# Optimization experiments

Hardware: AMD Instinct MI355X
Metric: run time of the kernel (lower is better)

Reference implementation:

```python
import jax, jax.numpy as jnp
import numpy as np

B, P, E, D = 256, 2048, 16, 2
HID, OUT = 128, 128
BN_EPS = 1e-5


def setup_inputs() -> dict:
    key = jax.random.key(0)
    ks = jax.random.split(key, 16)
    inp = {
        "barcode_h0": jax.random.normal(ks[0], (B, P, D), jnp.float32),
        "barcode_h0_count": jax.random.randint(ks[1], (B,), 0, P),
        "barcode_h1": jax.random.normal(ks[2], (B, P, D), jnp.float32),
        "barcode_h1_count": jax.random.randint(ks[3], (B,), 0, P),
        # SLayer params (one per homology dim): centers ~ U[0,1), log_sharpness = log(3.0)
        "centers0": jax.random.uniform(ks[4], (E, D), jnp.float32),
        "log_sharp0": jnp.full((E, D), np.log(3.0), jnp.float32),
        "centers1": jax.random.uniform(ks[5], (E, D), jnp.float32),
        "log_sharp1": jnp.full((E, D), np.log(3.0), jnp.float32),
        # head: Linear(2E -> HID, no bias), BN, ReLU, Linear(HID -> OUT, no bias), BN
        "W1": jax.random.normal(ks[6], (2 * E, HID), jnp.float32) / np.sqrt(2 * E),
        "gamma1": jnp.ones((HID,), jnp.float32),
        "beta1": jnp.zeros((HID,), jnp.float32),
        "W2": jax.random.normal(ks[7], (HID, OUT), jnp.float32) / np.sqrt(HID),
        "gamma2": jnp.ones((OUT,), jnp.float32),
        "beta2": jnp.zeros((OUT,), jnp.float32),
    }
    return inp


def _slayer(pts, counts, centers, log_sharp):
    # pts: [B,P,2], counts: [B], centers/log_sharp: [E,2]
    sharp = jax.nn.softplus(log_sharp) + 1e-6                       # [E,2]
    diff = pts[:, :, None, :] - centers[None, None, :, :]           # [B,P,E,2]
    resp = jnp.exp(-jnp.sum(sharp * diff * diff, axis=-1))          # [B,P,E]
    mask = (jnp.arange(pts.shape[1])[None, :] < counts[:, None]).astype(resp.dtype)
    return jnp.sum(resp * mask[:, :, None], axis=1)                 # [B,E]


def _batchnorm_train(x, gamma, beta):
    m = jnp.mean(x, axis=0)
    v = jnp.var(x, axis=0)  # biased, as torch uses for normalization
    return (x - m) * jax.lax.rsqrt(v + BN_EPS) * gamma + beta


def reference(barcode_h0, barcode_h0_count, barcode_h1, barcode_h1_count,
              centers0, log_sharp0, centers1, log_sharp1,
              W1, gamma1, beta1, W2, gamma2, beta2):
    f0 = _slayer(barcode_h0, barcode_h0_count, centers0, log_sharp0)  # [B,E]
    f1 = _slayer(barcode_h1, barcode_h1_count, centers1, log_sharp1)  # [B,E]
    x = jnp.concatenate([f0, f1], axis=1)                             # [B,2E]
    h = jax.nn.relu(_batchnorm_train(x @ W1, gamma1, beta1))          # [B,HID]
    y = _batchnorm_train(h @ W2, gamma2, beta2)                       # [B,OUT]
    norm = jnp.maximum(jnp.linalg.norm(y, axis=1, keepdims=True), 1e-12)
    return y / norm
```

## Files before the change

### kernel.cpp

```cpp
#include <hip/hip_runtime.h>

#define Bsz 256
#define Pn  2048
#define En  16
#define HIDn 128
#define OUTn 128
#define BN_EPS 1e-5f

__global__ __launch_bounds__(256) void k_slayer_w1(
    const float* __restrict__ pts0, const int* __restrict__ cnt0,
    const float* __restrict__ pts1, const int* __restrict__ cnt1,
    const float* __restrict__ c0, const float* __restrict__ ls0,
    const float* __restrict__ c1, const float* __restrict__ ls1,
    const float* __restrict__ W1,
    float* __restrict__ u, float* __restrict__ sum1, float* __restrict__ sumsq1)
{
    __shared__ float cen[2][En][2];
    __shared__ float shp[2][En][2];
    __shared__ float red[4][32];
    __shared__ float xrow[32];

    const int tid = threadIdx.x;
    const int b   = blockIdx.x;

    if (tid < 64) {
        int h = tid >> 5, r = tid & 31, e = r >> 1, d = r & 1;
        const float* C = h ? c1 : c0;
        const float* L = h ? ls1 : ls0;
        cen[h][e][d] = C[e * 2 + d];
        float z  = L[e * 2 + d];
        float sp = (z > 20.f) ? z : logf(1.f + expf(z));
        shp[h][e][d] = sp + 1e-6f;
    }
    __syncthreads();

    float acc0[En], acc1[En];
    #pragma unroll
    for (int e = 0; e < En; e++) { acc0[e] = 0.f; acc1[e] = 0.f; }

    const int n0 = cnt0[b];
    const int n1 = cnt1[b];
    const float2* p0 = (const float2*)pts0 + (size_t)b * Pn;
    const float2* p1 = (const float2*)pts1 + (size_t)b * Pn;

    for (int p = tid; p < n0; p += 256) {
        float2 pt = p0[p];
        #pragma unroll
        for (int e = 0; e < En; e++) {
            float dx = pt.x - cen[0][e][0];
            float dy = pt.y - cen[0][e][1];
            float t  = shp[0][e][0] * dx * dx + shp[0][e][1] * dy * dy;
            acc0[e] += __expf(-t);
        }
    }
    for (int p = tid; p < n1; p += 256) {
        float2 pt = p1[p];
        #pragma unroll
        for (int e = 0; e < En; e++) {
            float dx = pt.x - cen[1][e][0];
            float dy = pt.y - cen[1][e][1];
            float t  = shp[1][e][0] * dx * dx + shp[1][e][1] * dy * dy;
            acc1[e] += __expf(-t);
        }
    }

    #pragma unroll
    for (int e = 0; e < En; e++) {
        #pragma unroll
        for (int off = 32; off > 0; off >>= 1) {
            acc0[e] += __shfl_down(acc0[e], off, 64);
            acc1[e] += __shfl_down(acc1[e], off, 64);
        }
    }
    const int wave = tid >> 6, lane = tid & 63;
    if (lane == 0) {
        #pragma unroll
        for (int e = 0; e < En; e++) { red[wave][e] = acc0[e]; red[wave][16 + e] = acc1[e]; }
    }
    __syncthreads();
    if (tid < 32) xrow[tid] = red[0][tid] + red[1][tid] + red[2][tid] + red[3][tid];
    __syncthreads();

    if (tid < HIDn) {
        float a = 0.f;
        #pragma unroll
        for (int k = 0; k < 32; k++) a = fmaf(xrow[k], W1[k * HIDn + tid], a);
        u[b * HIDn + tid] = a;
        atomicAdd(&sum1[tid], a);
        atomicAdd(&sumsq1[tid], a * a);
    }
}

__global__ __launch_bounds__(128) void k_bn1_w2(
    const float* __restrict__ u, const float* __restrict__ W2,
    const float* __restrict__ g1, const float* __restrict__ be1,
    const float* __restrict__ sum1, const float* __restrict__ sumsq1,
    float* __restrict__ ypre, float* __restrict__ sum2, float* __restrict__ sumsq2)
{
    __shared__ float hrow[HIDn];
    const int j = threadIdx.x, b = blockIdx.x;

    float uv   = u[b * HIDn + j];
    float m    = sum1[j] * (1.f / Bsz);
    float var  = sumsq1[j] * (1.f / Bsz) - m * m;
    float rstd = rsqrtf(var + BN_EPS);
    float h    = fmaxf((uv - m) * rstd * g1[j] + be1[j], 0.f);
    hrow[j] = h;
    __syncthreads();

    float a = 0.f;
    #pragma unroll 8
    for (int k = 0; k < HIDn; k++) a = fmaf(hrow[k], W2[k * OUTn + j], a);

    ypre[b * OUTn + j] = a;
    atomicAdd(&sum2[j], a);
    atomicAdd(&sumsq2[j], a * a);
}

__global__ __launch_bounds__(128) void k_bn2_norm(
    const float* __restrict__ ypre,
    const float* __restrict__ g2, const float* __restrict__ be2,
    const float* __restrict__ sum2, const float* __restrict__ sumsq2,
    float* __restrict__ out)
{
    __shared__ float part[2];
    const int j = threadIdx.x, b = blockIdx.x;

    float yv   = ypre[b * OUTn + j];
    float m    = sum2[j] * (1.f / Bsz);
    float var  = sumsq2[j] * (1.f / Bsz) - m * m;
    float rstd = rsqrtf(var + BN_EPS);
    float y    = (yv - m) * rstd * g2[j] + be2[j];

    float sq = y * y;
    #pragma unroll
    for (int off = 32; off > 0; off >>= 1) sq += __shfl_down(sq, off, 64);
    if ((j & 63) == 0) part[j >> 6] = sq;
    __syncthreads();
    float total = part[0] + part[1];
    float norm  = fmaxf(sqrtf(total), 1e-12f);
    out[b * OUTn + j] = y / norm;
}

extern "C" void kernel_launch(void* const* d_in, const int* in_sizes, int n_in,
                              void* d_out, int out_size, void* d_ws, size_t ws_size,
                              hipStream_t stream) {
    const float* pts0 = (const float*)d_in[0];
    const int*   cnt0 = (const int*)  d_in[1];
    const float* pts1 = (const float*)d_in[2];
    const int*   cnt1 = (const int*)  d_in[3];
    const float* c0   = (const float*)d_in[4];
    const float* ls0  = (const float*)d_in[5];
    const float* c1   = (const float*)d_in[6];
    const float* ls1  = (const float*)d_in[7];
    const float* W1   = (const float*)d_in[8];
    const float* g1   = (const float*)d_in[9];
    const float* be1  = (const float*)d_in[10];
    const float* W2   = (const float*)d_in[11];
    const float* g2   = (const float*)d_in[12];
    const float* be2  = (const float*)d_in[13];
    float* out = (float*)d_out;

    float* ws     = (float*)d_ws;
    float* u      = ws;
    float* ypre   = ws + 32768;
    float* sum1   = ws + 65536;
    float* sumsq1 = sum1 + 128;
    float* sum2   = sumsq1 + 128;
    float* sumsq2 = sum2 + 128;

    hipMemsetAsync(sum1, 0, 512 * sizeof(float), stream);

    k_slayer_w1<<<Bsz, 256, 0, stream>>>(pts0, cnt0, pts1, cnt1,
                                         c0, ls0, c1, ls1, W1,
                                         u, sum1, sumsq1);
    k_bn1_w2<<<Bsz, 128, 0, stream>>>(u, W2, g1, be1, sum1, sumsq1,
                                      ypre, sum2, sumsq2);
    k_bn2_norm<<<Bsz, 128, 0, stream>>>(ypre, g2, be2, sum2, sumsq2, out);
}
```

Measured before the change: 106.9 us.

## Fuse three kernels into one cooperative kernel with grid syncs

```diff
diff --git a/kernel.cpp b/kernel.cpp
--- a/kernel.cpp
+++ b/kernel.cpp
@@ -1,4 +1,7 @@
 #include <hip/hip_runtime.h>
+#include <hip/hip_cooperative_groups.h>
+
+namespace cg = cooperative_groups;
 
 #define Bsz 256
 #define Pn  2048
@@ -7,18 +10,27 @@
 #define OUTn 128
 #define BN_EPS 1e-5f
 
-__global__ __launch_bounds__(256) void k_slayer_w1(
+__global__ __launch_bounds__(256) void k_fused(
     const float* __restrict__ pts0, const int* __restrict__ cnt0,
     const float* __restrict__ pts1, const int* __restrict__ cnt1,
     const float* __restrict__ c0, const float* __restrict__ ls0,
     const float* __restrict__ c1, const float* __restrict__ ls1,
     const float* __restrict__ W1,
-    float* __restrict__ u, float* __restrict__ sum1, float* __restrict__ sumsq1)
+    const float* __restrict__ g1, const float* __restrict__ be1,
+    const float* __restrict__ W2,
+    const float* __restrict__ g2, const float* __restrict__ be2,
+    float* __restrict__ sum1, float* __restrict__ sumsq1,
+    float* __restrict__ sum2, float* __restrict__ sumsq2,
+    float* __restrict__ out)
 {
+    cg::grid_group grid = cg::this_grid();
+
     __shared__ float cen[2][En][2];
     __shared__ float shp[2][En][2];
     __shared__ float red[4][32];
     __shared__ float xrow[32];
+    __shared__ float hrow[HIDn];
+    __shared__ float part[4];
 
     const int tid = threadIdx.x;
     const int b   = blockIdx.x;
@@ -81,65 +93,51 @@
     if (tid < 32) xrow[tid] = red[0][tid] + red[1][tid] + red[2][tid] + red[3][tid];
     __syncthreads();
 
+    float uv = 0.f;
     if (tid < HIDn) {
-        float a = 0.f;
         #pragma unroll
-        for (int k = 0; k < 32; k++) a = fmaf(xrow[k], W1[k * HIDn + tid], a);
-        u[b * HIDn + tid] = a;
-        atomicAdd(&sum1[tid], a);
-        atomicAdd(&sumsq1[tid], a * a);
+        for (int k = 0; k < 32; k++) uv = fmaf(xrow[k], W1[k * HIDn + tid], uv);
+        atomicAdd(&sum1[tid], uv);
+        atomicAdd(&sumsq1[tid], uv * uv);
     }
-}
 
-__global__ __launch_bounds__(128) void k_bn1_w2(
-    const float* __restrict__ u, const float* __restrict__ W2,
-    const float* __restrict__ g1, const float* __restrict__ be1,
-    const float* __restrict__ sum1, const float* __restrict__ sumsq1,
-    float* __restrict__ ypre, float* __restrict__ sum2, float* __restrict__ sumsq2)
-{
-    __shared__ float hrow[HIDn];
-    const int j = threadIdx.x, b = blockIdx.x;
+    grid.sync();
 
-    float uv   = u[b * HIDn + j];
-    float m    = sum1[j] * (1.f / Bsz);
-    float var  = sumsq1[j] * (1.f / Bsz) - m * m;
-    float rstd = rsqrtf(var + BN_EPS);
-    float h    = fmaxf((uv - m) * rstd * g1[j] + be1[j], 0.f);
-    hrow[j] = h;
+    if (tid < HIDn) {
+        float m    = sum1[tid] * (1.f / Bsz);
+        float var  = sumsq1[tid] * (1.f / Bsz) - m * m;
+        float rstd = rsqrtf(var + BN_EPS);
+        hrow[tid]  = fmaxf((uv - m) * rstd * g1[tid] + be1[tid], 0.f);
+    }
     __syncthreads();
 
     float a = 0.f;
-    #pragma unroll 8
-    for (int k = 0; k < HIDn; k++) a = fmaf(hrow[k], W2[k * OUTn + j], a);
+    if (tid < OUTn) {
+        #pragma unroll 8
+        for (int k = 0; k < HIDn; k++) a = fmaf(hrow[k], W2[k * OUTn + tid], a);
+        atomicAdd(&sum2[tid], a);
+        atomicAdd(&sumsq2[tid], a * a);
+    }
 
-    ypre[b * OUTn + j] = a;
-    atomicAdd(&sum2[j], a);
-    atomicAdd(&sumsq2[j], a * a);
-}
+    grid.sync();
 
-__global__ __launch_bounds__(128) void k_bn2_norm(
-    const float* __restrict__ ypre,
-    const float* __restrict__ g2, const float* __restrict__ be2,
-    const float* __restrict__ sum2, const float* __restrict__ sumsq2,
-    float* __restrict__ out)
-{
-    __shared__ float part[2];
-    const int j = threadIdx.x, b = blockIdx.x;
-
-    float yv   = ypre[b * OUTn + j];
-    float m    = sum2[j] * (1.f / Bsz);
-    float var  = sumsq2[j] * (1.f / Bsz) - m * m;
-    float rstd = rsqrtf(var + BN_EPS);
-    float y    = (yv - m) * rstd * g2[j] + be2[j];
-
+    float y = 0.f;
+    if (tid < OUTn) {
+        float m    = sum2[tid] * (1.f / Bsz);
+        float var  = sumsq2[tid] * (1.f / Bsz) - m * m;
+        float rstd = rsqrtf(var + BN_EPS);
+        y = (a - m) * rstd * g2[tid] + be2[tid];
+    }
     float sq = y * y;
     #pragma unroll
     for (int off = 32; off > 0; off >>= 1) sq += __shfl_down(sq, off, 64);
-    if ((j & 63) == 0) part[j >> 6] = sq;
+    if (lane == 0) part[wave] = sq;
     __syncthreads();
-    float total = part[0] + part[1];
-    float norm  = fmaxf(sqrtf(total), 1e-12f);
-    out[b * OUTn + j] = y / norm;
+    if (tid < OUTn) {
+        float total = part[0] + part[1] + part[2] + part[3];
+        float norm  = fmaxf(sqrtf(total), 1e-12f);
+        out[b * OUTn + tid] = y / norm;
+    }
 }
 
 extern "C" void kernel_launch(void* const* d_in, const int* in_sizes, int n_in,
@@ -162,19 +160,21 @@
     float* out = (float*)d_out;
 
     float* ws     = (float*)d_ws;
-    float* u      = ws;
-    float* ypre   = ws + 32768;
-    float* sum1   = ws + 65536;
-    float* sumsq1 = sum1 + 128;
-    float* sum2   = sumsq1 + 128;
-    float* sumsq2 = sum2 + 128;
+    float* sum1   = ws;
+    float* sumsq1 = ws + 128;
+    float* sum2   = ws + 256;
+    float* sumsq2 = ws + 384;
 
-    hipMemsetAsync(sum1, 0, 512 * sizeof(float), stream);
+    hipMemsetAsync(ws, 0, 512 * sizeof(float), stream);
 
-    k_slayer_w1<<<Bsz, 256, 0, stream>>>(pts0, cnt0, pts1, cnt1,
-                                         c0, ls0, c1, ls1, W1,
-                                         u, sum1, sumsq1);
-    k_bn1_w2<<<Bsz, 128, 0, stream>>>(u, W2, g1, be1, sum1, sumsq1,
-                                      ypre, sum2, sumsq2);
-    k_bn2_norm<<<Bsz, 128, 0, stream>>>(ypre, g2, be2, sum2, sumsq2, out);
+    void* args[] = {
+        (void*)&pts0, (void*)&cnt0, (void*)&pts1, (void*)&cnt1,
+        (void*)&c0, (void*)&ls0, (void*)&c1, (void*)&ls1,
+        (void*)&W1, (void*)&g1, (void*)&be1,
+        (void*)&W2, (void*)&g2, (void*)&be2,
+        (void*)&sum1, (void*)&sumsq1, (void*)&sum2, (void*)&sumsq2,
+        (void*)&out
+    };
+    hipLaunchCooperativeKernel((const void*)k_fused, dim3(Bsz), dim3(256),
+                               args, 0, stream);
 }
```

Measured after the change: 175.1 us. +63.7%, slower.
